# Kernel optimization log

Measured on AMD Instinct MI355X. Metric: run time of the kernel, lower is better.

The kernel has to match this reference:

```python
import jax, jax.numpy as jnp
import numpy as np

N = 65536
SIZES = [2, 256, 256, 256, 256, 256, 1]


def setup_inputs() -> dict:
    key = jax.random.key(0)
    ks = jax.random.split(key, 2 + 2 * (len(SIZES) - 1))
    d = {
        "vect": jax.random.normal(ks[0], (N, 2), dtype=jnp.float32),
        "vals": jax.random.randint(ks[1], (N,), 0, 3, dtype=jnp.int32),  # 0=interior,1=inlet,2=outlet
    }
    for i in range(len(SIZES) - 1):
        fan_in = SIZES[i]
        d[f"W{i}"] = jax.random.normal(ks[2 + i], (SIZES[i], SIZES[i + 1]), dtype=jnp.float32) / np.float32(np.sqrt(fan_in))
        d[f"b{i}"] = jnp.zeros((SIZES[i + 1],), dtype=jnp.float32)
    return d


def reference(vect, vals, W0, b0, W1, b1, W2, b2, W3, b3, W4, b4, W5, b5):
    Ws = [W0, W1, W2, W3, W4, W5]
    bs = [b0, b1, b2, b3, b4, b5]

    def net(p):  # p: [..., 2] -> [..., 1]
        h = p
        for W, b in zip(Ws[:-1], bs[:-1]):
            h = jnp.tanh(h @ W + b)
        return h @ Ws[-1] + bs[-1]

    # T(x, y) at all collocation points  -> [N]
    T = net(vect)[:, 0]

    # Laplacian T_xx + T_yy per point: trace of the 2x2 Hessian of the
    # scalar network (forward-over-reverse, vmapped over points).
    def f_scalar(pt):  # pt: [2] -> scalar
        return net(pt)[0]

    hess = jax.vmap(jax.hessian(f_scalar))(vect)  # [N, 2, 2]
    res_T = hess[:, 0, 0] + hess[:, 1, 1]          # [N]

    loss_res = jnp.mean(jnp.square(res_T))

    def masked_mse(mask, target):
        cnt = jnp.maximum(jnp.sum(mask.astype(jnp.float32)), 1.0)
        se = jnp.where(mask, jnp.square(T - target), 0.0)
        return jnp.sum(se) / cnt

    loss_inlet = masked_mse(vals == 1, 1200.0)
    loss_outlet = masked_mse(vals == 2, 25.0)

    loss = loss_res + loss_inlet + loss_outlet
    return loss
```

## Files before the change

kernel.cpp:

```cpp
#include <hip/hip_runtime.h>

#define N_PTS   65536
#define PBLK    32
#define NBLK    (N_PTS / PBLK)
#define HID     256
#define NCH     4

typedef __attribute__((ext_vector_type(16))) float floatx16;
typedef __attribute__((ext_vector_type(8)))  int   int8v;
typedef __attribute__((ext_vector_type(4)))  long long llx4;
typedef __attribute__((ext_vector_type(2)))  unsigned uint2v;

__device__ __forceinline__ float fast_tanh(float x) {
    float e = exp2f(2.885390082f * x);
    return 1.0f - 2.0f / (e + 1.0f);
}
__device__ __forceinline__ unsigned pk4_fp8(float a, float b, float c, float d) {
    unsigned w = __builtin_amdgcn_cvt_pk_fp8_f32(a, b, 0, false);
    w = __builtin_amdgcn_cvt_pk_fp8_f32(c, d, (int)w, true);
    return w;
}

__global__ __launch_bounds__(64) void conv_w(
    const float* __restrict__ W1, const float* __restrict__ W2,
    const float* __restrict__ W3, const float* __restrict__ W4,
    unsigned char* __restrict__ Wt)
{
    int layer = blockIdx.x >> 8;
    int n     = blockIdx.x & 255;
    const float* W = (layer == 0) ? W1 : (layer == 1) ? W2 : (layer == 2) ? W3 : W4;
    int t = threadIdx.x;
    float a = W[(t * 4 + 0) * 256 + n];
    float b = W[(t * 4 + 1) * 256 + n];
    float c = W[(t * 4 + 2) * 256 + n];
    float d = W[(t * 4 + 3) * 256 + n];
    ((unsigned*)Wt)[((layer << 8) + n) * 64 + t] = pk4_fp8(a, b, c, d);
}

__global__ __launch_bounds__(512, 4) void pinn_main(
    const float* __restrict__ vect, const int* __restrict__ vals,
    const float* __restrict__ W0, const float* __restrict__ b0,
    const float* __restrict__ b1, const float* __restrict__ b2,
    const float* __restrict__ b3, const float* __restrict__ b4,
    const float* __restrict__ W5, const float* __restrict__ b5,
    const unsigned char* __restrict__ Wt, float* __restrict__ partials)
{
    __shared__ __align__(16) unsigned char Hs[2][NCH][PBLK][HID];
    __shared__ float red[8][5];

    const int tid   = threadIdx.x;
    const int wave  = tid >> 6;
    const int lane  = tid & 63;
    const int pt    = lane & 31;
    const int hi    = lane >> 5;
    const int pbase = blockIdx.x * PBLK;
    const int swz   = (pt & 15) << 3;

    {
        const int p0 = tid & 31;
        const int c0 = (tid >> 5) * 16;
        const int sz = (p0 & 15) << 3;
        float x = vect[(pbase + p0) * 2 + 0];
        float y = vect[(pbase + p0) * 2 + 1];
        #pragma unroll
        for (int jj = 0; jj < 2; ++jj) {
            const int cb = c0 + jj * 8;
            float4 wxa = *(const float4*)(W0 + cb);
            float4 wxb = *(const float4*)(W0 + cb + 4);
            float4 wya = *(const float4*)(W0 + HID + cb);
            float4 wyb = *(const float4*)(W0 + HID + cb + 4);
            float4 bba = *(const float4*)(b0 + cb);
            float4 bbb = *(const float4*)(b0 + cb + 4);
            float wx[8] = {wxa.x, wxa.y, wxa.z, wxa.w, wxb.x, wxb.y, wxb.z, wxb.w};
            float wy[8] = {wya.x, wya.y, wya.z, wya.w, wyb.x, wyb.y, wyb.z, wyb.w};
            float bb[8] = {bba.x, bba.y, bba.z, bba.w, bbb.x, bbb.y, bbb.z, bbb.w};
            float av[8], pv[8], mv[8], hv[8];
            #pragma unroll
            for (int q = 0; q < 8; ++q) {
                float z  = x * wx[q] + y * wy[q] + bb[q];
                float a  = fast_tanh(z);
                float s  = 1.0f - a * a;
                float gx = s * wx[q];
                float gy = s * wy[q];
                av[q] = a;
                pv[q] = gx + gy;
                mv[q] = gx - gy;
                hv[q] = -2.0f * a * (gx * wx[q] + gy * wy[q]);
            }
            const int idx = p0 * 256 + (cb ^ sz);
            *(uint2v*)&Hs[0][0][0][idx] = (uint2v){pk4_fp8(av[0],av[1],av[2],av[3]),
                                                   pk4_fp8(av[4],av[5],av[6],av[7])};
            *(uint2v*)&Hs[0][1][0][idx] = (uint2v){pk4_fp8(pv[0],pv[1],pv[2],pv[3]),
                                                   pk4_fp8(pv[4],pv[5],pv[6],pv[7])};
            *(uint2v*)&Hs[0][2][0][idx] = (uint2v){pk4_fp8(mv[0],mv[1],mv[2],mv[3]),
                                                   pk4_fp8(mv[4],mv[5],mv[6],mv[7])};
            *(uint2v*)&Hs[0][3][0][idx] = (uint2v){pk4_fp8(hv[0],hv[1],hv[2],hv[3]),
                                                   pk4_fp8(hv[4],hv[5],hv[6],hv[7])};
        }
    }
    __syncthreads();

    const float* bs[4] = {b1, b2, b3, b4};

    floatx16 zk = (floatx16)(0.0f);

    #pragma unroll
    for (int L = 0; L < 4; ++L) {
        const int cur = L & 1;
        const int nxt = cur ^ 1;
        floatx16 acc[NCH];

        const unsigned char* wb = Wt + L * 65536 + (((wave << 5) + pt) << 8) + (hi << 5);
        const unsigned char* hb = &Hs[cur][0][pt][0];

        __builtin_amdgcn_s_setprio(1);
        #pragma unroll
        for (int ks4 = 0; ks4 < 4; ++ks4) {
            const int kb = ks4 * 64 + (hi << 5);
            int4 a0 = *(const int4*)(wb + ks4 * 64);
            int4 a1 = *(const int4*)(wb + ks4 * 64 + 16);
            int8v af;
            af[0] = a0.x; af[1] = a0.y; af[2] = a0.z; af[3] = a0.w;
            af[4] = a1.x; af[5] = a1.y; af[6] = a1.z; af[7] = a1.w;
            #pragma unroll
            for (int ch = 0; ch < NCH; ++ch) {
                llx4 t;
                t[0] = *(const long long*)(hb + ch * 8192 + ((kb +  0) ^ swz));
                t[1] = *(const long long*)(hb + ch * 8192 + ((kb +  8) ^ swz));
                t[2] = *(const long long*)(hb + ch * 8192 + ((kb + 16) ^ swz));
                t[3] = *(const long long*)(hb + ch * 8192 + ((kb + 24) ^ swz));
                int8v bfv = __builtin_bit_cast(int8v, t);
                acc[ch] = __builtin_amdgcn_mfma_scale_f32_32x32x64_f8f6f4(
                    af, bfv, (ks4 == 0) ? zk : acc[ch], 0, 0, 0, 0x7F, 0, 0x7F);
            }
        }
        __builtin_amdgcn_s_setprio(0);

        unsigned char* hw = &Hs[nxt][0][pt][0];
        #pragma unroll
        for (int q = 0; q < 4; ++q) {
            const int nq = (wave << 5) + q * 8 + hi * 4;
            float4 bb4 = *(const float4*)(bs[L] + nq);
            float bb[4] = {bb4.x, bb4.y, bb4.z, bb4.w};
            float av[4], pv[4], mv[4], hv[4];
            #pragma unroll
            for (int r = 0; r < 4; ++r) {
                const int reg = q * 4 + r;
                float z  = acc[0][reg] + bb[r];
                float a  = fast_tanh(z);
                float s  = 1.0f - a * a;
                float zp = acc[1][reg];
                float zm = acc[2][reg];
                float zh = acc[3][reg];
                av[r] = a;
                pv[r] = s * zp;
                mv[r] = s * zm;
                hv[r] = s * zh - a * s * (zp * zp + zm * zm);
            }
            const int kk = nq ^ swz;
            *(unsigned*)(hw + 0 * 8192 + kk) = pk4_fp8(av[0], av[1], av[2], av[3]);
            *(unsigned*)(hw + 1 * 8192 + kk) = pk4_fp8(pv[0], pv[1], pv[2], pv[3]);
            *(unsigned*)(hw + 2 * 8192 + kk) = pk4_fp8(mv[0], mv[1], mv[2], mv[3]);
            *(unsigned*)(hw + 3 * 8192 + kk) = pk4_fp8(hv[0], hv[1], hv[2], hv[3]);
        }
        __syncthreads();
    }

    const int fp  = (wave << 2) + (lane >> 4);
    const int kc  = (lane & 15) * 16;
    const int fsz = (fp & 15) << 3;
    float sT = 0.f, sR = 0.f;
    #pragma unroll
    for (int j = 0; j < 2; ++j) {
        const int kb = kc + j * 8;
        const int ke = kb ^ fsz;
        uint2v hv = *(const uint2v*)(&Hs[0][0][fp][0] + ke);
        uint2v hh = *(const uint2v*)(&Hs[0][3][fp][0] + ke);
        float4 w5a = *(const float4*)(W5 + kb);
        float4 w5b = *(const float4*)(W5 + kb + 4);
        sT += __builtin_amdgcn_cvt_f32_fp8((int)hv.x, 0) * w5a.x
            + __builtin_amdgcn_cvt_f32_fp8((int)hv.x, 1) * w5a.y
            + __builtin_amdgcn_cvt_f32_fp8((int)hv.x, 2) * w5a.z
            + __builtin_amdgcn_cvt_f32_fp8((int)hv.x, 3) * w5a.w
            + __builtin_amdgcn_cvt_f32_fp8((int)hv.y, 0) * w5b.x
            + __builtin_amdgcn_cvt_f32_fp8((int)hv.y, 1) * w5b.y
            + __builtin_amdgcn_cvt_f32_fp8((int)hv.y, 2) * w5b.z
            + __builtin_amdgcn_cvt_f32_fp8((int)hv.y, 3) * w5b.w;
        sR += __builtin_amdgcn_cvt_f32_fp8((int)hh.x, 0) * w5a.x
            + __builtin_amdgcn_cvt_f32_fp8((int)hh.x, 1) * w5a.y
            + __builtin_amdgcn_cvt_f32_fp8((int)hh.x, 2) * w5a.z
            + __builtin_amdgcn_cvt_f32_fp8((int)hh.x, 3) * w5a.w
            + __builtin_amdgcn_cvt_f32_fp8((int)hh.y, 0) * w5b.x
            + __builtin_amdgcn_cvt_f32_fp8((int)hh.y, 1) * w5b.y
            + __builtin_amdgcn_cvt_f32_fp8((int)hh.y, 2) * w5b.z
            + __builtin_amdgcn_cvt_f32_fp8((int)hh.y, 3) * w5b.w;
    }
    sT += __shfl_down(sT, 8, 64); sR += __shfl_down(sR, 8, 64);
    sT += __shfl_down(sT, 4, 64); sR += __shfl_down(sR, 4, 64);
    sT += __shfl_down(sT, 2, 64); sR += __shfl_down(sR, 2, 64);
    sT += __shfl_down(sT, 1, 64); sR += __shfl_down(sR, 1, 64);

    float r0 = 0.f, r1 = 0.f, r2 = 0.f, r3 = 0.f, r4 = 0.f;
    if ((lane & 15) == 0) {
        float T = sT + b5[0];
        r0 = sR * sR;
        int m = vals[pbase + fp];
        if (m == 1)      { float d = T - 1200.0f; r1 = d * d; r2 = 1.0f; }
        else if (m == 2) { float d = T - 25.0f;   r3 = d * d; r4 = 1.0f; }
    }
    #pragma unroll
    for (int off = 32; off >= 16; off >>= 1) {
        r0 += __shfl_down(r0, off, 64);
        r1 += __shfl_down(r1, off, 64);
        r2 += __shfl_down(r2, off, 64);
        r3 += __shfl_down(r3, off, 64);
        r4 += __shfl_down(r4, off, 64);
    }
    if (lane == 0) {
        red[wave][0] = r0; red[wave][1] = r1; red[wave][2] = r2;
        red[wave][3] = r3; red[wave][4] = r4;
    }
    __syncthreads();
    if (tid == 0) {
        #pragma unroll
        for (int c = 0; c < 5; ++c) {
            float s = 0.f;
            #pragma unroll
            for (int w = 0; w < 8; ++w) s += red[w][c];
            partials[blockIdx.x * 5 + c] = s;
        }
    }
}

__global__ __launch_bounds__(256) void pinn_reduce(const float* __restrict__ p,
                                                   float* __restrict__ out)
{
    float s[5] = {0.f, 0.f, 0.f, 0.f, 0.f};
    for (int idx = threadIdx.x; idx < NBLK; idx += 256) {
        #pragma unroll
        for (int c = 0; c < 5; ++c) s[c] += p[idx * 5 + c];
    }
    #pragma unroll
    for (int c = 0; c < 5; ++c) {
        #pragma unroll
        for (int off = 32; off > 0; off >>= 1)
            s[c] += __shfl_down(s[c], off, 64);
    }
    __shared__ float r[4][5];
    int wave = threadIdx.x >> 6;
    int lane = threadIdx.x & 63;
    if (lane == 0) {
        #pragma unroll
        for (int c = 0; c < 5; ++c) r[wave][c] = s[c];
    }
    __syncthreads();
    if (threadIdx.x == 0) {
        float t[5];
        #pragma unroll
        for (int c = 0; c < 5; ++c) t[c] = r[0][c] + r[1][c] + r[2][c] + r[3][c];
        out[0] = t[0] / (float)N_PTS
               + t[1] / fmaxf(t[2], 1.0f)
               + t[3] / fmaxf(t[4], 1.0f);
    }
}

extern "C" void kernel_launch(void* const* d_in, const int* in_sizes, int n_in,
                              void* d_out, int out_size, void* d_ws, size_t ws_size,
                              hipStream_t stream) {
    const float* vect = (const float*)d_in[0];
    const int*   vals = (const int*)d_in[1];
    const float* W0 = (const float*)d_in[2];
    const float* b0 = (const float*)d_in[3];
    const float* W1 = (const float*)d_in[4];
    const float* b1 = (const float*)d_in[5];
    const float* W2 = (const float*)d_in[6];
    const float* b2 = (const float*)d_in[7];
    const float* W3 = (const float*)d_in[8];
    const float* b3 = (const float*)d_in[9];
    const float* W4 = (const float*)d_in[10];
    const float* b4 = (const float*)d_in[11];
    const float* W5 = (const float*)d_in[12];
    const float* b5 = (const float*)d_in[13];

    float* partials    = (float*)d_ws;
    unsigned char* Wt  = (unsigned char*)d_ws + 131072;
    float* out         = (float*)d_out;

    conv_w<<<1024, 64, 0, stream>>>(W1, W2, W3, W4, Wt);
    pinn_main<<<NBLK, 512, 0, stream>>>(vect, vals, W0, b0, b1, b2, b3, b4,
                                        W5, b5, Wt, partials);
    pinn_reduce<<<1, 256, 0, stream>>>(partials, out);
}
```

Baseline: 135.1 us.

## Switch to 16-point blocks using 16x16x128 FP8 MFMA tiles

Halves the points per block from 32 to 16 and replaces the 32x32x64 scaled FP8 MFMA with 16x16x128, with each wave computing two 16-row output tiles per channel. The shared-memory layout, swizzle, layer-0 setup and final reduction are reworked to match, and the occupancy hint rises from 4 to 6 blocks per SM. The goal is more blocks and less shared memory per block for better latency hiding and more waves per CU. In exchange, each weight fragment is reused across fewer points, so weight traffic from L2 per point doubles.

```diff
diff --git a/kernel.cpp b/kernel.cpp
--- a/kernel.cpp
+++ b/kernel.cpp
@@ -1,14 +1,13 @@
 #include <hip/hip_runtime.h>
 
 #define N_PTS   65536
-#define PBLK    32
+#define PBLK    16
 #define NBLK    (N_PTS / PBLK)
 #define HID     256
 #define NCH     4
 
-typedef __attribute__((ext_vector_type(16))) float floatx16;
+typedef __attribute__((ext_vector_type(4)))  float floatx4;
 typedef __attribute__((ext_vector_type(8)))  int   int8v;
-typedef __attribute__((ext_vector_type(4)))  long long llx4;
 typedef __attribute__((ext_vector_type(2)))  unsigned uint2v;
 
 __device__ __forceinline__ float fast_tanh(float x) {
@@ -19,6 +18,12 @@
     unsigned w = __builtin_amdgcn_cvt_pk_fp8_f32(a, b, 0, false);
     w = __builtin_amdgcn_cvt_pk_fp8_f32(c, d, (int)w, true);
     return w;
+}
+__device__ __forceinline__ int8v mk8(int4 a, int4 b) {
+    int8v v;
+    v[0] = a.x; v[1] = a.y; v[2] = a.z; v[3] = a.w;
+    v[4] = b.x; v[5] = b.y; v[6] = b.z; v[7] = b.w;
+    return v;
 }
 
 __global__ __launch_bounds__(64) void conv_w(
@@ -37,7 +42,7 @@
     ((unsigned*)Wt)[((layer << 8) + n) * 64 + t] = pk4_fp8(a, b, c, d);
 }
 
-__global__ __launch_bounds__(512, 4) void pinn_main(
+__global__ __launch_bounds__(512, 6) void pinn_main(
     const float* __restrict__ vect, const int* __restrict__ vals,
     const float* __restrict__ W0, const float* __restrict__ b0,
     const float* __restrict__ b1, const float* __restrict__ b2,
@@ -51,171 +56,158 @@
     const int tid   = threadIdx.x;
     const int wave  = tid >> 6;
     const int lane  = tid & 63;
-    const int pt    = lane & 31;
-    const int hi    = lane >> 5;
+    const int pt    = lane & 15;
+    const int g     = lane >> 4;
     const int pbase = blockIdx.x * PBLK;
-    const int swz   = (pt & 15) << 3;
+    const int swz   = pt << 4;
 
     {
-        const int p0 = tid & 31;
-        const int c0 = (tid >> 5) * 16;
-        const int sz = (p0 & 15) << 3;
+        const int p0 = tid >> 5;
+        const int c0 = (tid & 31) * 8;
+        const int sz = (p0 & 15) << 4;
         float x = vect[(pbase + p0) * 2 + 0];
         float y = vect[(pbase + p0) * 2 + 1];
-        #pragma unroll
-        for (int jj = 0; jj < 2; ++jj) {
-            const int cb = c0 + jj * 8;
-            float4 wxa = *(const float4*)(W0 + cb);
-            float4 wxb = *(const float4*)(W0 + cb + 4);
-            float4 wya = *(const float4*)(W0 + HID + cb);
-            float4 wyb = *(const float4*)(W0 + HID + cb + 4);
-            float4 bba = *(const float4*)(b0 + cb);
-            float4 bbb = *(const float4*)(b0 + cb + 4);
-            float wx[8] = {wxa.x, wxa.y, wxa.z, wxa.w, wxb.x, wxb.y, wxb.z, wxb.w};
-            float wy[8] = {wya.x, wya.y, wya.z, wya.w, wyb.x, wyb.y, wyb.z, wyb.w};
-            float bb[8] = {bba.x, bba.y, bba.z, bba.w, bbb.x, bbb.y, bbb.z, bbb.w};
-            float av[8], pv[8], mv[8], hv[8];
-            #pragma unroll
-            for (int q = 0; q < 8; ++q) {
-                float z  = x * wx[q] + y * wy[q] + bb[q];
-                float a  = fast_tanh(z);
-                float s  = 1.0f - a * a;
-                float gx = s * wx[q];
-                float gy = s * wy[q];
-                av[q] = a;
-                pv[q] = gx + gy;
-                mv[q] = gx - gy;
-                hv[q] = -2.0f * a * (gx * wx[q] + gy * wy[q]);
-            }
-            const int idx = p0 * 256 + (cb ^ sz);
-            *(uint2v*)&Hs[0][0][0][idx] = (uint2v){pk4_fp8(av[0],av[1],av[2],av[3]),
-                                                   pk4_fp8(av[4],av[5],av[6],av[7])};
-            *(uint2v*)&Hs[0][1][0][idx] = (uint2v){pk4_fp8(pv[0],pv[1],pv[2],pv[3]),
-                                                   pk4_fp8(pv[4],pv[5],pv[6],pv[7])};
-            *(uint2v*)&Hs[0][2][0][idx] = (uint2v){pk4_fp8(mv[0],mv[1],mv[2],mv[3]),
-                                                   pk4_fp8(mv[4],mv[5],mv[6],mv[7])};
-            *(uint2v*)&Hs[0][3][0][idx] = (uint2v){pk4_fp8(hv[0],hv[1],hv[2],hv[3]),
-                                                   pk4_fp8(hv[4],hv[5],hv[6],hv[7])};
-        }
+        float4 wxa = *(const float4*)(W0 + c0);
+        float4 wxb = *(const float4*)(W0 + c0 + 4);
+        float4 wya = *(const float4*)(W0 + HID + c0);
+        float4 wyb = *(const float4*)(W0 + HID + c0 + 4);
+        float4 bba = *(const float4*)(b0 + c0);
+        float4 bbb = *(const float4*)(b0 + c0 + 4);
+        float wx[8] = {wxa.x, wxa.y, wxa.z, wxa.w, wxb.x, wxb.y, wxb.z, wxb.w};
+        float wy[8] = {wya.x, wya.y, wya.z, wya.w, wyb.x, wyb.y, wyb.z, wyb.w};
+        float bb[8] = {bba.x, bba.y, bba.z, bba.w, bbb.x, bbb.y, bbb.z, bbb.w};
+        float av[8], pv[8], mv[8], hv[8];
+        #pragma unroll
+        for (int q = 0; q < 8; ++q) {
+            float z  = x * wx[q] + y * wy[q] + bb[q];
+            float a  = fast_tanh(z);
+            float s  = 1.0f - a * a;
+            float gx = s * wx[q];
+            float gy = s * wy[q];
+            av[q] = a;
+            pv[q] = gx + gy;
+            mv[q] = gx - gy;
+            hv[q] = -2.0f * a * (gx * wx[q] + gy * wy[q]);
+        }
+        const int idx = p0 * 256 + (c0 ^ sz);
+        *(uint2v*)&Hs[0][0][0][idx] = (uint2v){pk4_fp8(av[0],av[1],av[2],av[3]),
+                                               pk4_fp8(av[4],av[5],av[6],av[7])};
+        *(uint2v*)&Hs[0][1][0][idx] = (uint2v){pk4_fp8(pv[0],pv[1],pv[2],pv[3]),
+                                               pk4_fp8(pv[4],pv[5],pv[6],pv[7])};
+        *(uint2v*)&Hs[0][2][0][idx] = (uint2v){pk4_fp8(mv[0],mv[1],mv[2],mv[3]),
+                                               pk4_fp8(mv[4],mv[5],mv[6],mv[7])};
+        *(uint2v*)&Hs[0][3][0][idx] = (uint2v){pk4_fp8(hv[0],hv[1],hv[2],hv[3]),
+                                               pk4_fp8(hv[4],hv[5],hv[6],hv[7])};
     }
     __syncthreads();
 
     const float* bs[4] = {b1, b2, b3, b4};
 
-    floatx16 zk = (floatx16)(0.0f);
+    floatx4 zk = (floatx4){0.f, 0.f, 0.f, 0.f};
 
     #pragma unroll
     for (int L = 0; L < 4; ++L) {
         const int cur = L & 1;
         const int nxt = cur ^ 1;
-        floatx16 acc[NCH];
-
-        const unsigned char* wb = Wt + L * 65536 + (((wave << 5) + pt) << 8) + (hi << 5);
-        const unsigned char* hb = &Hs[cur][0][pt][0];
+        floatx4 acc[2][NCH];
+
+        const unsigned char* wb = Wt + L * 65536 + ((wave << 5) + pt) * 256 + (g << 5);
+        const unsigned char* hb = &Hs[cur][0][0][0];
 
         __builtin_amdgcn_s_setprio(1);
         #pragma unroll
-        for (int ks4 = 0; ks4 < 4; ++ks4) {
-            const int kb = ks4 * 64 + (hi << 5);
-            int4 a0 = *(const int4*)(wb + ks4 * 64);
-            int4 a1 = *(const int4*)(wb + ks4 * 64 + 16);
-            int8v af;
-            af[0] = a0.x; af[1] = a0.y; af[2] = a0.z; af[3] = a0.w;
-            af[4] = a1.x; af[5] = a1.y; af[6] = a1.z; af[7] = a1.w;
+        for (int kst = 0; kst < 2; ++kst) {
+            const int kb = kst * 128 + (g << 5);
+            int8v af0 = mk8(*(const int4*)(wb + kst * 128),
+                            *(const int4*)(wb + kst * 128 + 16));
+            int8v af1 = mk8(*(const int4*)(wb + 16 * 256 + kst * 128),
+                            *(const int4*)(wb + 16 * 256 + kst * 128 + 16));
             #pragma unroll
             for (int ch = 0; ch < NCH; ++ch) {
-                llx4 t;
-                t[0] = *(const long long*)(hb + ch * 8192 + ((kb +  0) ^ swz));
-                t[1] = *(const long long*)(hb + ch * 8192 + ((kb +  8) ^ swz));
-                t[2] = *(const long long*)(hb + ch * 8192 + ((kb + 16) ^ swz));
-                t[3] = *(const long long*)(hb + ch * 8192 + ((kb + 24) ^ swz));
-                int8v bfv = __builtin_bit_cast(int8v, t);
-                acc[ch] = __builtin_amdgcn_mfma_scale_f32_32x32x64_f8f6f4(
-                    af, bfv, (ks4 == 0) ? zk : acc[ch], 0, 0, 0, 0x7F, 0, 0x7F);
+                const unsigned char* hc = hb + ch * 4096 + pt * 256;
+                int8v bfv = mk8(*(const int4*)(hc + ((kb +  0) ^ swz)),
+                                *(const int4*)(hc + ((kb + 16) ^ swz)));
+                acc[0][ch] = __builtin_amdgcn_mfma_scale_f32_16x16x128_f8f6f4(
+                    af0, bfv, (kst == 0) ? zk : acc[0][ch], 0, 0, 0, 0x7F, 0, 0x7F);
+                acc[1][ch] = __builtin_amdgcn_mfma_scale_f32_16x16x128_f8f6f4(
+                    af1, bfv, (kst == 0) ? zk : acc[1][ch], 0, 0, 0, 0x7F, 0, 0x7F);
             }
         }
         __builtin_amdgcn_s_setprio(0);
 
-        unsigned char* hw = &Hs[nxt][0][pt][0];
-        #pragma unroll
-        for (int q = 0; q < 4; ++q) {
-            const int nq = (wave << 5) + q * 8 + hi * 4;
+        unsigned char* hw = &Hs[nxt][0][0][0];
+        #pragma unroll
+        for (int t = 0; t < 2; ++t) {
+            const int nq = (wave << 5) + t * 16 + (g << 2);
             float4 bb4 = *(const float4*)(bs[L] + nq);
             float bb[4] = {bb4.x, bb4.y, bb4.z, bb4.w};
             float av[4], pv[4], mv[4], hv[4];
             #pragma unroll
             for (int r = 0; r < 4; ++r) {
-                const int reg = q * 4 + r;
-                float z  = acc[0][reg] + bb[r];
+                float z  = acc[t][0][r] + bb[r];
                 float a  = fast_tanh(z);
                 float s  = 1.0f - a * a;
-                float zp = acc[1][reg];
-                float zm = acc[2][reg];
-                float zh = acc[3][reg];
+                float zp = acc[t][1][r];
+                float zm = acc[t][2][r];
+                float zh = acc[t][3][r];
                 av[r] = a;
                 pv[r] = s * zp;
                 mv[r] = s * zm;
                 hv[r] = s * zh - a * s * (zp * zp + zm * zm);
             }
-            const int kk = nq ^ swz;
-            *(unsigned*)(hw + 0 * 8192 + kk) = pk4_fp8(av[0], av[1], av[2], av[3]);
-            *(unsigned*)(hw + 1 * 8192 + kk) = pk4_fp8(pv[0], pv[1], pv[2], pv[3]);
-            *(unsigned*)(hw + 2 * 8192 + kk) = pk4_fp8(mv[0], mv[1], mv[2], mv[3]);
-            *(unsigned*)(hw + 3 * 8192 + kk) = pk4_fp8(hv[0], hv[1], hv[2], hv[3]);
+            const int kk = pt * 256 + (nq ^ swz);
+            *(unsigned*)(hw + 0 * 4096 + kk) = pk4_fp8(av[0], av[1], av[2], av[3]);
+            *(unsigned*)(hw + 1 * 4096 + kk) = pk4_fp8(pv[0], pv[1], pv[2], pv[3]);
+            *(unsigned*)(hw + 2 * 4096 + kk) = pk4_fp8(mv[0], mv[1], mv[2], mv[3]);
+            *(unsigned*)(hw + 3 * 4096 + kk) = pk4_fp8(hv[0], hv[1], hv[2], hv[3]);
         }
         __syncthreads();
     }
 
-    const int fp  = (wave << 2) + (lane >> 4);
-    const int kc  = (lane & 15) * 16;
-    const int fsz = (fp & 15) << 3;
-    float sT = 0.f, sR = 0.f;
-    #pragma unroll
-    for (int j = 0; j < 2; ++j) {
-        const int kb = kc + j * 8;
-        const int ke = kb ^ fsz;
-        uint2v hv = *(const uint2v*)(&Hs[0][0][fp][0] + ke);
-        uint2v hh = *(const uint2v*)(&Hs[0][3][fp][0] + ke);
-        float4 w5a = *(const float4*)(W5 + kb);
-        float4 w5b = *(const float4*)(W5 + kb + 4);
-        sT += __builtin_amdgcn_cvt_f32_fp8((int)hv.x, 0) * w5a.x
-            + __builtin_amdgcn_cvt_f32_fp8((int)hv.x, 1) * w5a.y
-            + __builtin_amdgcn_cvt_f32_fp8((int)hv.x, 2) * w5a.z
-            + __builtin_amdgcn_cvt_f32_fp8((int)hv.x, 3) * w5a.w
-            + __builtin_amdgcn_cvt_f32_fp8((int)hv.y, 0) * w5b.x
-            + __builtin_amdgcn_cvt_f32_fp8((int)hv.y, 1) * w5b.y
-            + __builtin_amdgcn_cvt_f32_fp8((int)hv.y, 2) * w5b.z
-            + __builtin_amdgcn_cvt_f32_fp8((int)hv.y, 3) * w5b.w;
-        sR += __builtin_amdgcn_cvt_f32_fp8((int)hh.x, 0) * w5a.x
-            + __builtin_amdgcn_cvt_f32_fp8((int)hh.x, 1) * w5a.y
-            + __builtin_amdgcn_cvt_f32_fp8((int)hh.x, 2) * w5a.z
-            + __builtin_amdgcn_cvt_f32_fp8((int)hh.x, 3) * w5a.w
-            + __builtin_amdgcn_cvt_f32_fp8((int)hh.y, 0) * w5b.x
-            + __builtin_amdgcn_cvt_f32_fp8((int)hh.y, 1) * w5b.y
-            + __builtin_amdgcn_cvt_f32_fp8((int)hh.y, 2) * w5b.z
-            + __builtin_amdgcn_cvt_f32_fp8((int)hh.y, 3) * w5b.w;
-    }
-    sT += __shfl_down(sT, 8, 64); sR += __shfl_down(sR, 8, 64);
-    sT += __shfl_down(sT, 4, 64); sR += __shfl_down(sR, 4, 64);
-    sT += __shfl_down(sT, 2, 64); sR += __shfl_down(sR, 2, 64);
-    sT += __shfl_down(sT, 1, 64); sR += __shfl_down(sR, 1, 64);
+    const int fp  = (wave << 1) + (lane >> 5);
+    const int kc  = (lane & 31) * 8;
+    const int fsz = (fp & 15) << 4;
+    const int ke  = fp * 256 + (kc ^ fsz);
+    uint2v hv = *(const uint2v*)&Hs[0][0][0][ke];
+    uint2v hh = *(const uint2v*)&Hs[0][3][0][ke];
+    float4 w5a = *(const float4*)(W5 + kc);
+    float4 w5b = *(const float4*)(W5 + kc + 4);
+    float sT, sR;
+    sT = __builtin_amdgcn_cvt_f32_fp8((int)hv.x, 0) * w5a.x
+       + __builtin_amdgcn_cvt_f32_fp8((int)hv.x, 1) * w5a.y
+       + __builtin_amdgcn_cvt_f32_fp8((int)hv.x, 2) * w5a.z
+       + __builtin_amdgcn_cvt_f32_fp8((int)hv.x, 3) * w5a.w
+       + __builtin_amdgcn_cvt_f32_fp8((int)hv.y, 0) * w5b.x
+       + __builtin_amdgcn_cvt_f32_fp8((int)hv.y, 1) * w5b.y
+       + __builtin_amdgcn_cvt_f32_fp8((int)hv.y, 2) * w5b.z
+       + __builtin_amdgcn_cvt_f32_fp8((int)hv.y, 3) * w5b.w;
+    sR = __builtin_amdgcn_cvt_f32_fp8((int)hh.x, 0) * w5a.x
+       + __builtin_amdgcn_cvt_f32_fp8((int)hh.x, 1) * w5a.y
+       + __builtin_amdgcn_cvt_f32_fp8((int)hh.x, 2) * w5a.z
+       + __builtin_amdgcn_cvt_f32_fp8((int)hh.x, 3) * w5a.w
+       + __builtin_amdgcn_cvt_f32_fp8((int)hh.y, 0) * w5b.x
+       + __builtin_amdgcn_cvt_f32_fp8((int)hh.y, 1) * w5b.y
+       + __builtin_amdgcn_cvt_f32_fp8((int)hh.y, 2) * w5b.z
+       + __builtin_amdgcn_cvt_f32_fp8((int)hh.y, 3) * w5b.w;
+    sT += __shfl_down(sT, 16, 64); sR += __shfl_down(sR, 16, 64);
+    sT += __shfl_down(sT,  8, 64); sR += __shfl_down(sR,  8, 64);
+    sT += __shfl_down(sT,  4, 64); sR += __shfl_down(sR,  4, 64);
+    sT += __shfl_down(sT,  2, 64); sR += __shfl_down(sR,  2, 64);
+    sT += __shfl_down(sT,  1, 64); sR += __shfl_down(sR,  1, 64);
 
     float r0 = 0.f, r1 = 0.f, r2 = 0.f, r3 = 0.f, r4 = 0.f;
-    if ((lane & 15) == 0) {
+    if ((lane & 31) == 0) {
         float T = sT + b5[0];
         r0 = sR * sR;
         int m = vals[pbase + fp];
         if (m == 1)      { float d = T - 1200.0f; r1 = d * d; r2 = 1.0f; }
         else if (m == 2) { float d = T - 25.0f;   r3 = d * d; r4 = 1.0f; }
     }
-    #pragma unroll
-    for (int off = 32; off >= 16; off >>= 1) {
-        r0 += __shfl_down(r0, off, 64);
-        r1 += __shfl_down(r1, off, 64);
-        r2 += __shfl_down(r2, off, 64);
-        r3 += __shfl_down(r3, off, 64);
-        r4 += __shfl_down(r4, off, 64);
-    }
+    r0 += __shfl_down(r0, 32, 64);
+    r1 += __shfl_down(r1, 32, 64);
+    r2 += __shfl_down(r2, 32, 64);
+    r3 += __shfl_down(r3, 32, 64);
+    r4 += __shfl_down(r4, 32, 64);
     if (lane == 0) {
         red[wave][0] = r0; red[wave][1] = r1; red[wave][2] = r2;
         red[wave][3] = r3; red[wave][4] = r4;
```

After: 182.9 us. +35.4%, slower.
